# Kernel optimization log

Hardware: AMD Instinct MI355X
Metric: run time of the kernel (lower is better)

The kernel has to match this reference:

```python
import jax, jax.numpy as jnp
import numpy as np

B, N, DIM = 4, 2048, 512
HEADS, DK = 8, 64
SCALE = DK ** -0.5


def setup_inputs() -> dict:
    key = jax.random.key(0)
    k1, k2, k3, k4 = jax.random.split(key, 4)
    x = jax.random.normal(k1, (B, N, DIM), dtype=jnp.float32)
    # nn.Linear(dim, dim_key*heads, bias=False): y = x @ W.T; store W already transposed
    Wq = jax.random.normal(k2, (DIM, HEADS * DK), dtype=jnp.float32) * (DIM ** -0.5)
    Wk = jax.random.normal(k3, (DIM, HEADS * DK), dtype=jnp.float32) * (DIM ** -0.5)
    rel_content_bias = jax.random.normal(k4, (1, HEADS, 1, DK), dtype=jnp.float32)
    return {"x": x, "Wq": Wq, "Wk": Wk, "rel_content_bias": rel_content_bias}


def _split_heads(t, h):
    # [b, n, h*d] -> [b, h, n, d]
    b, n, hd = t.shape
    return t.reshape(b, n, h, hd // h).transpose(0, 2, 1, 3)


def reference(x, Wq, Wk, rel_content_bias):
    q = _split_heads(x @ Wq, HEADS) * SCALE          # [b, h, n, dk]
    k = _split_heads(x @ Wk, HEADS)                  # [b, h, n, dk]
    v = _split_heads(x, HEADS)                       # [b, h, n, dim/h]
    logits = jnp.einsum('bhid,bhjd->bhij', q + rel_content_bias, k)
    attn = jax.nn.sigmoid(logits)                    # no softmax normalization
    out = jnp.einsum('bhij,bhjd->bhid', attn, v)     # [b, h, n, dim/h]
    b, h, n, d = out.shape
    return out.transpose(0, 2, 1, 3).reshape(b, n, h * d)
```

## Files before the change

kernel.cpp:

```cpp
#include <hip/hip_runtime.h>
#include <hip/hip_bf16.h>
#include <stdint.h>

#define BB 4
#define NN 2048
#define DIMD 512
#define HH 8
#define DKK 64
#define MTOT (BB * NN)
constexpr float SCALE = 0.125f;

typedef __attribute__((ext_vector_type(4))) float f32x4;
typedef __attribute__((ext_vector_type(8))) short bf16x8;

__device__ __forceinline__ unsigned short f2bf(float f) {
  union { float f; uint32_t u; } v; v.f = f;
  uint32_t u = v.u;
  return (unsigned short)((u + 0x7FFFu + ((u >> 16) & 1u)) >> 16);
}

__device__ __forceinline__ float fast_sigmoid(float x) {
  return __builtin_amdgcn_rcpf(1.0f + __expf(-x));
}

__global__ __launch_bounds__(256) void prep_x(const float* __restrict__ x,
                                              unsigned short* __restrict__ xb,
                                              unsigned short* __restrict__ xt) {
  __shared__ __align__(16) unsigned short T[64][72];
  const int b = blockIdx.z, nt = blockIdx.x, dt = blockIdx.y;
  const int tid = threadIdx.x;
  const int n0 = nt * 64, d0 = dt * 64;
  const float* src = x + ((size_t)b * NN + n0) * DIMD + d0;
#pragma unroll
  for (int r = 0; r < 16; r++) {
    int idx = tid + r * 256;
    int nl = idx >> 6, dl = idx & 63;
    unsigned short bv = f2bf(src[(size_t)nl * DIMD + dl]);
    xb[((size_t)b * NN + n0 + nl) * DIMD + d0 + dl] = bv;
    T[dl][nl] = bv;
  }
  __syncthreads();
  unsigned short* dst = xt + ((size_t)b * DIMD + d0) * NN + n0;
#pragma unroll
  for (int r = 0; r < 16; r++) {
    int idx = tid + r * 256;
    int dl = idx >> 6, nl = idx & 63;
    dst[(size_t)dl * NN + nl] = T[dl][nl];
  }
}

__global__ __launch_bounds__(256) void prep_w(const float* __restrict__ w,
                                              unsigned short* __restrict__ wt) {
  __shared__ __align__(16) unsigned short T[64][72];
  const int kt = blockIdx.x, nt = blockIdx.y;
  const int tid = threadIdx.x;
  const int k0 = kt * 64, n0 = nt * 64;
#pragma unroll
  for (int r = 0; r < 16; r++) {
    int idx = tid + r * 256;
    int kl = idx >> 6, nl = idx & 63;
    T[nl][kl] = f2bf(w[(size_t)(k0 + kl) * DIMD + n0 + nl]);
  }
  __syncthreads();
#pragma unroll
  for (int r = 0; r < 16; r++) {
    int idx = tid + r * 256;
    int nl = idx >> 6, kl = idx & 63;
    wt[(size_t)(n0 + nl) * DIMD + k0 + kl] = T[nl][kl];
  }
}

__global__ __launch_bounds__(256) void qk_gemm(const unsigned short* __restrict__ xb,
                                               const unsigned short* __restrict__ wtq,
                                               const unsigned short* __restrict__ wtk,
                                               const float* __restrict__ bias,
                                               unsigned short* __restrict__ qout,
                                               unsigned short* __restrict__ kout) {
  __shared__ __align__(16) unsigned short Als[64][72];
  __shared__ __align__(16) unsigned short Bls[64][72];
  const int mb = blockIdx.x, nb = blockIdx.y;
  const bool isQ = (nb < 8);
  const unsigned short* wt = isQ ? wtq : wtk;
  unsigned short* out = isQ ? qout : kout;
  const int n0 = (nb & 7) * 64;
  const int m0 = mb * 64;
  const int tid = threadIdx.x;
  const int wave = tid >> 6, lane = tid & 63;
  const int quad = lane >> 4, l16 = lane & 15;

  f32x4 acc[4];
#pragma unroll
  for (int t = 0; t < 4; t++) acc[t] = (f32x4){0.f, 0.f, 0.f, 0.f};

  for (int k0 = 0; k0 < DIMD; k0 += 64) {
    __syncthreads();
#pragma unroll
    for (int r = 0; r < 2; r++) {
      int idx = tid + r * 256;
      int row = idx >> 3, c = idx & 7;
      *(uint4*)&Als[row][c * 8] =
          *(const uint4*)(xb + (size_t)(m0 + row) * DIMD + k0 + c * 8);
      *(uint4*)&Bls[row][c * 8] =
          *(const uint4*)(wt + (size_t)(n0 + row) * DIMD + k0 + c * 8);
    }
    __syncthreads();
#pragma unroll
    for (int ks = 0; ks < 2; ks++) {
      bf16x8 af = *(const bf16x8*)&Als[wave * 16 + l16][quad * 8 + ks * 32];
#pragma unroll
      for (int t = 0; t < 4; t++) {
        bf16x8 bf = *(const bf16x8*)&Bls[t * 16 + l16][quad * 8 + ks * 32];
        acc[t] = __builtin_amdgcn_mfma_f32_16x16x32_bf16(af, bf, acc[t], 0, 0, 0);
      }
    }
  }
#pragma unroll
  for (int t = 0; t < 4; t++) {
#pragma unroll
    for (int r = 0; r < 4; r++) {
      int row = m0 + wave * 16 + quad * 4 + r;
      int col = n0 + t * 16 + l16;
      float v = acc[t][r];
      if (isQ) v = v * SCALE + bias[col];
      out[(size_t)row * DIMD + col] = f2bf(v);
    }
  }
}

__global__ __launch_bounds__(256) void attn(const unsigned short* __restrict__ qb,
                                            const unsigned short* __restrict__ kb,
                                            const unsigned short* __restrict__ xt,
                                            float* __restrict__ out) {
  __shared__ __align__(16) unsigned short Kls[64][72];
  __shared__ __align__(16) unsigned short Vtls[64][72];
  __shared__ __align__(16) unsigned short Pls[4][16][72];
  const int it = blockIdx.x, bh = blockIdx.y;
  const int b = bh >> 3, h = bh & 7;
  const int i0 = it * 64;
  const int tid = threadIdx.x;
  const int wave = tid >> 6, lane = tid & 63;
  const int quad = lane >> 4, l16 = lane & 15;

  bf16x8 qfrag[2];
  {
    const unsigned short* qp =
        qb + ((size_t)b * NN + i0 + wave * 16 + l16) * DIMD + h * DKK + quad * 8;
    qfrag[0] = *(const bf16x8*)qp;
    qfrag[1] = *(const bf16x8*)(qp + 32);
  }

  f32x4 o[4];
#pragma unroll
  for (int t = 0; t < 4; t++) o[t] = (f32x4){0.f, 0.f, 0.f, 0.f};

  const unsigned short* kbase = kb + (size_t)b * NN * DIMD + h * DKK;
  const unsigned short* vtbase = xt + ((size_t)b * DIMD + h * DKK) * NN;

  for (int j0 = 0; j0 < NN; j0 += 64) {
    __syncthreads();
#pragma unroll
    for (int r = 0; r < 2; r++) {
      int idx = tid + r * 256;
      int row = idx >> 3, c = idx & 7;
      *(uint4*)&Kls[row][c * 8] =
          *(const uint4*)(kbase + (size_t)(j0 + row) * DIMD + c * 8);
      *(uint4*)&Vtls[row][c * 8] =
          *(const uint4*)(vtbase + (size_t)row * NN + j0 + c * 8);
    }
    __syncthreads();

#pragma unroll
    for (int t = 0; t < 4; t++) {
      f32x4 s = (f32x4){0.f, 0.f, 0.f, 0.f};
      bf16x8 b0 = *(const bf16x8*)&Kls[t * 16 + l16][quad * 8];
      s = __builtin_amdgcn_mfma_f32_16x16x32_bf16(qfrag[0], b0, s, 0, 0, 0);
      bf16x8 b1 = *(const bf16x8*)&Kls[t * 16 + l16][quad * 8 + 32];
      s = __builtin_amdgcn_mfma_f32_16x16x32_bf16(qfrag[1], b1, s, 0, 0, 0);
#pragma unroll
      for (int r = 0; r < 4; r++) {
        Pls[wave][quad * 4 + r][t * 16 + l16] = f2bf(fast_sigmoid(s[r]));
      }
    }

#pragma unroll
    for (int ks = 0; ks < 2; ks++) {
      bf16x8 pf = *(const bf16x8*)&Pls[wave][l16][ks * 32 + quad * 8];
#pragma unroll
      for (int td = 0; td < 4; td++) {
        bf16x8 vf = *(const bf16x8*)&Vtls[td * 16 + l16][ks * 32 + quad * 8];
        o[td] = __builtin_amdgcn_mfma_f32_16x16x32_bf16(pf, vf, o[td], 0, 0, 0);
      }
    }
  }

#pragma unroll
  for (int td = 0; td < 4; td++) {
#pragma unroll
    for (int r = 0; r < 4; r++) {
      int row = i0 + wave * 16 + quad * 4 + r;
      out[((size_t)b * NN + row) * DIMD + h * DKK + td * 16 + l16] = o[td][r];
    }
  }
}

extern "C" void kernel_launch(void* const* d_in, const int* in_sizes, int n_in,
                              void* d_out, int out_size, void* d_ws, size_t ws_size,
                              hipStream_t stream) {
  const float* x = (const float*)d_in[0];
  const float* Wq = (const float*)d_in[1];
  const float* Wk = (const float*)d_in[2];
  const float* bias = (const float*)d_in[3];
  float* out = (float*)d_out;

  unsigned short* ws = (unsigned short*)d_ws;
  unsigned short* xb = ws;
  unsigned short* xt = xb + (size_t)MTOT * DIMD;
  unsigned short* wtq = xt + (size_t)MTOT * DIMD;
  unsigned short* wtk = wtq + (size_t)DIMD * DIMD;
  unsigned short* qb = wtk + (size_t)DIMD * DIMD;
  unsigned short* kb = qb + (size_t)MTOT * DIMD;

  prep_x<<<dim3(32, 8, 4), 256, 0, stream>>>(x, xb, xt);
  prep_w<<<dim3(8, 8), 256, 0, stream>>>(Wq, wtq);
  prep_w<<<dim3(8, 8), 256, 0, stream>>>(Wk, wtk);
  qk_gemm<<<dim3(128, 16), 256, 0, stream>>>(xb, wtq, wtk, bias, qb, kb);
  attn<<<dim3(32, 32), 256, 0, stream>>>(qb, kb, xt, out);
}
```

Before: 184.7 us.

## Keep sigmoid probabilities in registers with fp16 MFMA, enlarge GEMM and attention tiles

Result: faster. 180.2 us (-2.5%).

```diff
diff --git a/kernel.cpp b/kernel.cpp
--- a/kernel.cpp
+++ b/kernel.cpp
@@ -12,6 +12,9 @@
 
 typedef __attribute__((ext_vector_type(4))) float f32x4;
 typedef __attribute__((ext_vector_type(8))) short bf16x8;
+typedef __attribute__((ext_vector_type(4))) _Float16 f16x4;
+typedef __attribute__((ext_vector_type(2))) __fp16 fp16v2;
+typedef __attribute__((ext_vector_type(4))) __fp16 fp16v4;
 
 __device__ __forceinline__ unsigned short f2bf(float f) {
   union { float f; uint32_t u; } v; v.f = f;
@@ -19,13 +22,13 @@
   return (unsigned short)((u + 0x7FFFu + ((u >> 16) & 1u)) >> 16);
 }
 
-__device__ __forceinline__ float fast_sigmoid(float x) {
+__device__ __forceinline__ float sigmoidf(float x) {
   return __builtin_amdgcn_rcpf(1.0f + __expf(-x));
 }
 
 __global__ __launch_bounds__(256) void prep_x(const float* __restrict__ x,
                                               unsigned short* __restrict__ xb,
-                                              unsigned short* __restrict__ xt) {
+                                              unsigned short* __restrict__ xtf) {
   __shared__ __align__(16) unsigned short T[64][72];
   const int b = blockIdx.z, nt = blockIdx.x, dt = blockIdx.y;
   const int tid = threadIdx.x;
@@ -35,12 +38,13 @@
   for (int r = 0; r < 16; r++) {
     int idx = tid + r * 256;
     int nl = idx >> 6, dl = idx & 63;
-    unsigned short bv = f2bf(src[(size_t)nl * DIMD + dl]);
-    xb[((size_t)b * NN + n0 + nl) * DIMD + d0 + dl] = bv;
-    T[dl][nl] = bv;
+    float f = src[(size_t)nl * DIMD + dl];
+    xb[((size_t)b * NN + n0 + nl) * DIMD + d0 + dl] = f2bf(f);
+    union { _Float16 h; unsigned short u; } c; c.h = (_Float16)f;
+    T[dl][nl] = c.u;
   }
   __syncthreads();
-  unsigned short* dst = xt + ((size_t)b * DIMD + d0) * NN + n0;
+  unsigned short* dst = xtf + ((size_t)b * DIMD + d0) * NN + n0;
 #pragma unroll
   for (int r = 0; r < 16; r++) {
     int idx = tid + r * 256;
@@ -49,9 +53,13 @@
   }
 }
 
-__global__ __launch_bounds__(256) void prep_w(const float* __restrict__ w,
-                                              unsigned short* __restrict__ wt) {
+__global__ __launch_bounds__(256) void prep_w(const float* __restrict__ wq,
+                                              const float* __restrict__ wk,
+                                              unsigned short* __restrict__ wtq,
+                                              unsigned short* __restrict__ wtk) {
   __shared__ __align__(16) unsigned short T[64][72];
+  const float* w = blockIdx.z ? wk : wq;
+  unsigned short* wt = blockIdx.z ? wtk : wtq;
   const int kt = blockIdx.x, nt = blockIdx.y;
   const int tid = threadIdx.x;
   const int k0 = kt * 64, n0 = nt * 64;
@@ -76,26 +84,28 @@
                                                const float* __restrict__ bias,
                                                unsigned short* __restrict__ qout,
                                                unsigned short* __restrict__ kout) {
-  __shared__ __align__(16) unsigned short Als[64][72];
-  __shared__ __align__(16) unsigned short Bls[64][72];
+  __shared__ __align__(16) unsigned short Als[128][72];
+  __shared__ __align__(16) unsigned short Bls[128][72];
   const int mb = blockIdx.x, nb = blockIdx.y;
-  const bool isQ = (nb < 8);
+  const bool isQ = (nb < 4);
   const unsigned short* wt = isQ ? wtq : wtk;
-  unsigned short* out = isQ ? qout : kout;
-  const int n0 = (nb & 7) * 64;
-  const int m0 = mb * 64;
+  unsigned short* outp = isQ ? qout : kout;
+  const int n0 = (nb & 3) * 128, m0 = mb * 128;
   const int tid = threadIdx.x;
   const int wave = tid >> 6, lane = tid & 63;
   const int quad = lane >> 4, l16 = lane & 15;
-
-  f32x4 acc[4];
-#pragma unroll
-  for (int t = 0; t < 4; t++) acc[t] = (f32x4){0.f, 0.f, 0.f, 0.f};
+  const int wm = wave >> 1, wn = wave & 1;
+
+  f32x4 acc[4][4];
+#pragma unroll
+  for (int a = 0; a < 4; a++)
+#pragma unroll
+    for (int c = 0; c < 4; c++) acc[a][c] = (f32x4){0.f, 0.f, 0.f, 0.f};
 
   for (int k0 = 0; k0 < DIMD; k0 += 64) {
     __syncthreads();
 #pragma unroll
-    for (int r = 0; r < 2; r++) {
+    for (int r = 0; r < 4; r++) {
       int idx = tid + r * 256;
       int row = idx >> 3, c = idx & 7;
       *(uint4*)&Als[row][c * 8] =
@@ -106,55 +116,68 @@
     __syncthreads();
 #pragma unroll
     for (int ks = 0; ks < 2; ks++) {
-      bf16x8 af = *(const bf16x8*)&Als[wave * 16 + l16][quad * 8 + ks * 32];
+      bf16x8 af[4], bfr[4];
 #pragma unroll
       for (int t = 0; t < 4; t++) {
-        bf16x8 bf = *(const bf16x8*)&Bls[t * 16 + l16][quad * 8 + ks * 32];
-        acc[t] = __builtin_amdgcn_mfma_f32_16x16x32_bf16(af, bf, acc[t], 0, 0, 0);
-      }
-    }
-  }
-#pragma unroll
-  for (int t = 0; t < 4; t++) {
-#pragma unroll
-    for (int r = 0; r < 4; r++) {
-      int row = m0 + wave * 16 + quad * 4 + r;
-      int col = n0 + t * 16 + l16;
-      float v = acc[t][r];
-      if (isQ) v = v * SCALE + bias[col];
-      out[(size_t)row * DIMD + col] = f2bf(v);
+        af[t] = *(const bf16x8*)&Als[wm * 64 + t * 16 + l16][quad * 8 + ks * 32];
+        bfr[t] = *(const bf16x8*)&Bls[wn * 64 + t * 16 + l16][quad * 8 + ks * 32];
+      }
+#pragma unroll
+      for (int tm = 0; tm < 4; tm++)
+#pragma unroll
+        for (int tn = 0; tn < 4; tn++)
+          acc[tm][tn] =
+              __builtin_amdgcn_mfma_f32_16x16x32_bf16(af[tm], bfr[tn], acc[tm][tn], 0, 0, 0);
+    }
+  }
+#pragma unroll
+  for (int tm = 0; tm < 4; tm++) {
+#pragma unroll
+    for (int tn = 0; tn < 4; tn++) {
+#pragma unroll
+      for (int r = 0; r < 4; r++) {
+        int row = m0 + wm * 64 + tm * 16 + quad * 4 + r;
+        int gcol = n0 + wn * 64 + tn * 16 + l16;
+        float v = acc[tm][tn][r];
+        if (isQ) v = v * SCALE + bias[gcol];
+        outp[(size_t)row * DIMD + gcol] = f2bf(v);
+      }
     }
   }
 }
 
 __global__ __launch_bounds__(256) void attn(const unsigned short* __restrict__ qb,
                                             const unsigned short* __restrict__ kb,
-                                            const unsigned short* __restrict__ xt,
+                                            const unsigned short* __restrict__ xtf,
                                             float* __restrict__ out) {
   __shared__ __align__(16) unsigned short Kls[64][72];
   __shared__ __align__(16) unsigned short Vtls[64][72];
-  __shared__ __align__(16) unsigned short Pls[4][16][72];
   const int it = blockIdx.x, bh = blockIdx.y;
   const int b = bh >> 3, h = bh & 7;
-  const int i0 = it * 64;
+  const int i0 = it * 128;
   const int tid = threadIdx.x;
   const int wave = tid >> 6, lane = tid & 63;
   const int quad = lane >> 4, l16 = lane & 15;
 
-  bf16x8 qfrag[2];
-  {
+  bf16x8 qfrag[2][2];
+  int irow[2];
+#pragma unroll
+  for (int s_ = 0; s_ < 2; s_++) {
+    irow[s_] = i0 + (wave * 2 + s_) * 16 + l16;
     const unsigned short* qp =
-        qb + ((size_t)b * NN + i0 + wave * 16 + l16) * DIMD + h * DKK + quad * 8;
-    qfrag[0] = *(const bf16x8*)qp;
-    qfrag[1] = *(const bf16x8*)(qp + 32);
-  }
-
-  f32x4 o[4];
-#pragma unroll
-  for (int t = 0; t < 4; t++) o[t] = (f32x4){0.f, 0.f, 0.f, 0.f};
+        qb + ((size_t)b * NN + irow[s_]) * DIMD + h * DKK + quad * 8;
+    qfrag[s_][0] = *(const bf16x8*)qp;
+    qfrag[s_][1] = *(const bf16x8*)(qp + 32);
+  }
+
+  f32x4 o[2][4];
+#pragma unroll
+  for (int s_ = 0; s_ < 2; s_++)
+#pragma unroll
+    for (int td = 0; td < 4; td++) o[s_][td] = (f32x4){0.f, 0.f, 0.f, 0.f};
 
   const unsigned short* kbase = kb + (size_t)b * NN * DIMD + h * DKK;
-  const unsigned short* vtbase = xt + ((size_t)b * DIMD + h * DKK) * NN;
+  const unsigned short* vbase = xtf + ((size_t)b * DIMD + h * DKK) * NN;
 
   for (int j0 = 0; j0 < NN; j0 += 64) {
     __syncthreads();
@@ -165,40 +188,45 @@
       *(uint4*)&Kls[row][c * 8] =
           *(const uint4*)(kbase + (size_t)(j0 + row) * DIMD + c * 8);
       *(uint4*)&Vtls[row][c * 8] =
-          *(const uint4*)(vtbase + (size_t)row * NN + j0 + c * 8);
-    }
-    __syncthreads();
-
+          *(const uint4*)(vbase + (size_t)row * NN + j0 + c * 8);
+    }
+    __syncthreads();
+
+    f16x4 pfrag[2][4];
 #pragma unroll
     for (int t = 0; t < 4; t++) {
-      f32x4 s = (f32x4){0.f, 0.f, 0.f, 0.f};
-      bf16x8 b0 = *(const bf16x8*)&Kls[t * 16 + l16][quad * 8];
-      s = __builtin_amdgcn_mfma_f32_16x16x32_bf16(qfrag[0], b0, s, 0, 0, 0);
-      bf16x8 b1 = *(const bf16x8*)&Kls[t * 16 + l16][quad * 8 + 32];
-      s = __builtin_amdgcn_mfma_f32_16x16x32_bf16(qfrag[1], b1, s, 0, 0, 0);
-#pragma unroll
-      for (int r = 0; r < 4; r++) {
-        Pls[wave][quad * 4 + r][t * 16 + l16] = f2bf(fast_sigmoid(s[r]));
-      }
-    }
-
-#pragma unroll
-    for (int ks = 0; ks < 2; ks++) {
-      bf16x8 pf = *(const bf16x8*)&Pls[wave][l16][ks * 32 + quad * 8];
-#pragma unroll
-      for (int td = 0; td < 4; td++) {
-        bf16x8 vf = *(const bf16x8*)&Vtls[td * 16 + l16][ks * 32 + quad * 8];
-        o[td] = __builtin_amdgcn_mfma_f32_16x16x32_bf16(pf, vf, o[td], 0, 0, 0);
-      }
-    }
-  }
-
-#pragma unroll
-  for (int td = 0; td < 4; td++) {
-#pragma unroll
-    for (int r = 0; r < 4; r++) {
-      int row = i0 + wave * 16 + quad * 4 + r;
-      out[((size_t)b * NN + row) * DIMD + h * DKK + td * 16 + l16] = o[td][r];
+      bf16x8 kf0 = *(const bf16x8*)&Kls[t * 16 + l16][quad * 8];
+      bf16x8 kf1 = *(const bf16x8*)&Kls[t * 16 + l16][quad * 8 + 32];
+#pragma unroll
+      for (int s_ = 0; s_ < 2; s_++) {
+        f32x4 sv = (f32x4){0.f, 0.f, 0.f, 0.f};
+        sv = __builtin_amdgcn_mfma_f32_16x16x32_bf16(kf0, qfrag[s_][0], sv, 0, 0, 0);
+        sv = __builtin_amdgcn_mfma_f32_16x16x32_bf16(kf1, qfrag[s_][1], sv, 0, 0, 0);
+        fp16v2 lo = __builtin_amdgcn_cvt_pkrtz(sigmoidf(sv[0]), sigmoidf(sv[1]));
+        fp16v2 hi = __builtin_amdgcn_cvt_pkrtz(sigmoidf(sv[2]), sigmoidf(sv[3]));
+        fp16v4 p;
+        p.x = lo.x; p.y = lo.y; p.z = hi.x; p.w = hi.y;
+        pfrag[s_][t] = __builtin_bit_cast(f16x4, p);
+      }
+    }
+
+#pragma unroll
+    for (int td = 0; td < 4; td++) {
+#pragma unroll
+      for (int t = 0; t < 4; t++) {
+        f16x4 vf = *(const f16x4*)&Vtls[td * 16 + l16][t * 16 + quad * 4];
+        o[0][td] = __builtin_amdgcn_mfma_f32_16x16x16f16(vf, pfrag[0][t], o[0][td], 0, 0, 0);
+        o[1][td] = __builtin_amdgcn_mfma_f32_16x16x16f16(vf, pfrag[1][t], o[1][td], 0, 0, 0);
+      }
+    }
+  }
+
+#pragma unroll
+  for (int s_ = 0; s_ < 2; s_++) {
+#pragma unroll
+    for (int td = 0; td < 4; td++) {
+      float* op = out + ((size_t)b * NN + irow[s_]) * DIMD + h * DKK + td * 16 + quad * 4;
+      *(f32x4*)op = o[s_][td];
     }
   }
 }
@@ -214,15 +242,14 @@
 
   unsigned short* ws = (unsigned short*)d_ws;
   unsigned short* xb = ws;
-  unsigned short* xt = xb + (size_t)MTOT * DIMD;
-  unsigned short* wtq = xt + (size_t)MTOT * DIMD;
+  unsigned short* xtf = xb + (size_t)MTOT * DIMD;
+  unsigned short* wtq = xtf + (size_t)MTOT * DIMD;
   unsigned short* wtk = wtq + (size_t)DIMD * DIMD;
   unsigned short* qb = wtk + (size_t)DIMD * DIMD;
   unsigned short* kb = qb + (size_t)MTOT * DIMD;
 
-  prep_x<<<dim3(32, 8, 4), 256, 0, stream>>>(x, xb, xt);
-  prep_w<<<dim3(8, 8), 256, 0, stream>>>(Wq, wtq);
-  prep_w<<<dim3(8, 8), 256, 0, stream>>>(Wk, wtk);
-  qk_gemm<<<dim3(128, 16), 256, 0, stream>>>(xb, wtq, wtk, bias, qb, kb);
-  attn<<<dim3(32, 32), 256, 0, stream>>>(qb, kb, xt, out);
-}
+  prep_x<<<dim3(32, 8, 4), 256, 0, stream>>>(x, xb, xtf);
+  prep_w<<<dim3(8, 8, 2), 256, 0, stream>>>(Wq, Wk, wtq, wtk);
+  qk_gemm<<<dim3(64, 8), 256, 0, stream>>>(xb, wtq, wtk, bias, qb, kb);
+  attn<<<dim3(16, 32), 256, 0, stream>>>(qb, kb, xtf, out);
+}
```
